# Kernel tuning notes

Measured on AMD Instinct MI355X. Metric: run time of the kernel, lower is better.

## Reference

```python
import jax, jax.numpy as jnp
import numpy as np

LMBDA = 1.0
GAMMA = 1
TOL = 1e-4
MAX_ITER = 1000
MIN_REL_DIFFERENCE = 1e-5
M = 16_777_216  # number of per-example losses


def setup_inputs() -> dict:
    key = jax.random.key(0)
    v = jax.random.normal(key, (M,), dtype=jnp.float32)
    return {"v": v}


def _find_q(v):
    """Best-response distribution q over losses (lmbda > 0 branch)."""
    m = v.shape[0]
    mf = jnp.asarray(m, v.dtype)
    # size = lmbda^2 * Var(v)^(2*gamma - 1), unbiased variance (torch default)
    size = (LMBDA ** 2) * jnp.var(v, ddof=1) ** (2 * GAMMA - 1)
    vmax = jnp.max(v)
    vmin = jnp.min(v)

    def f(eta):
        pp = jax.nn.relu(v - eta)
        pp = pp / jnp.sum(pp)
        w = mf * pp - 1.0
        return jnp.mean(w * w) - size

    eta_min = -(1.0 / (jnp.sqrt(2.0 * size + 1.0) - 1.0)) * vmax
    eta_max = vmax

    # --- expansion phase: grow [eta_min, eta_max] until it brackets the root ---
    def exp_cond(s):
        _, _, lo, up = s
        return (lo > 0) | (up < 0)

    def exp_body(s):
        emin, emax, lo, up = s
        length = emax - emin
        emax1 = jnp.where(lo > 0, emin, emax)
        emin1 = jnp.where(lo > 0, emin - 2.0 * length, emin)
        emin2 = jnp.where(up < 0, emax1, emin1)
        emax2 = jnp.where(up < 0, emax1 + 2.0 * length, emax1)
        return emin2, emax2, f(emin2), f(emax2)

    emin, emax, _, _ = jax.lax.while_loop(
        exp_cond, exp_body, (eta_min, eta_max, f(eta_min), f(eta_max))
    )

    # --- bisection on increasing f ---
    def bis_cond(s):
        _, _, _, val, i = s
        return (jnp.abs(val) > TOL) & (i < MAX_ITER)

    def bis_body(s):
        bmin, bmax, eta, val, i = s
        bmax1 = jnp.where(val > 0, eta, bmax)
        bmin1 = jnp.where(val < 0, eta, bmin)
        eta1 = 0.5 * (bmin1 + bmax1)
        return bmin1, bmax1, eta1, f(eta1), i + 1

    eta0 = 0.5 * (emin + emax)
    _, _, eta_star, _, _ = jax.lax.while_loop(
        bis_cond, bis_body, (emin, emax, eta0, f(eta0), jnp.int32(1))
    )

    pp = jax.nn.relu(v - eta_star)
    q_bis = pp / jnp.sum(pp)

    # degenerate-case fallbacks (faithful to torch branches)
    q_uniform = jnp.full_like(v, 1.0 / mf)
    q_max = (v == vmax).astype(v.dtype)
    q_max = q_max / jnp.sum(q_max)

    cond_flat = (vmax - vmin) / vmax <= MIN_REL_DIFFERENCE
    cond_small = mf <= 1.0 + 2.0 * size
    return jnp.where(cond_flat, q_uniform, jnp.where(cond_small, q_max, q_bis))


def reference(v):
    # prob is computed without gradients in the original (torch.no_grad)
    prob = _find_q(jax.lax.stop_gradient(v))
    return jnp.dot(prob, v)
```

## Files before the change

kernel.cpp:

```cpp
#include <hip/hip_runtime.h>
#include <cfloat>
#include <limits.h>
#include <math.h>


#define NBINS   4096
#define BIN_LO  (-8.0)
#define BIN_W   (1.0/256.0)
#define BPB     512
#define K1T     1024

__global__ __launch_bounds__(1024)
void k1_hist_stats(const float* __restrict__ v, int n4,
                   unsigned int* __restrict__ pcnt,
                   unsigned int* __restrict__ Cnt32,
                   float* __restrict__ pmin, float* __restrict__ pmax,
                   double* __restrict__ psum, double* __restrict__ pssq)
{
    __shared__ unsigned int hc[NBINS];
    __shared__ float rmn[16], rmx[16];
    __shared__ double rs[16], rsq[16];
    const int tid = threadIdx.x;
    for (int i = tid; i < NBINS; i += K1T) hc[i] = 0u;
    if (blockIdx.x == 0) {
        for (int i = tid; i < NBINS; i += K1T) Cnt32[i] = 0u;
    }
    __syncthreads();

    const float4* __restrict__ v4 = (const float4*)v;
    float vmn = FLT_MAX, vmx = -FLT_MAX;
    double s = 0.0, sq = 0.0;
    const int stride = gridDim.x * K1T;
    for (int i = blockIdx.x * K1T + tid; i < n4; i += stride) {
        float4 x = v4[i];
        float cs[4] = {x.x, x.y, x.z, x.w};
        #pragma unroll
        for (int k = 0; k < 4; ++k) {
            float c = cs[k];
            vmn = fminf(vmn, c); vmx = fmaxf(vmx, c);
            s += (double)c; sq += (double)c * (double)c;
            int b = (int)floorf((c - (float)BIN_LO) * 256.0f);
            b = b < 0 ? 0 : (b > NBINS - 1 ? NBINS - 1 : b);
            atomicAdd(&hc[b], 1u);
        }
    }
    __syncthreads();
    const int base = blockIdx.x * NBINS;
    for (int i = tid; i < NBINS; i += K1T) pcnt[base + i] = hc[i];
    for (int off = 32; off > 0; off >>= 1) {
        vmn = fminf(vmn, __shfl_down(vmn, off));
        vmx = fmaxf(vmx, __shfl_down(vmx, off));
        s  += __shfl_down(s, off);
        sq += __shfl_down(sq, off);
    }
    const int lane = tid & 63, wid = tid >> 6;
    if (lane == 0) { rmn[wid] = vmn; rmx[wid] = vmx; rs[wid] = s; rsq[wid] = sq; }
    __syncthreads();
    if (tid == 0) {
        float a = rmn[0], b2 = rmx[0]; double c = rs[0], d = rsq[0];
        for (int i = 1; i < 16; ++i) { a = fminf(a, rmn[i]); b2 = fmaxf(b2, rmx[i]); c += rs[i]; d += rsq[i]; }
        pmin[blockIdx.x] = a; pmax[blockIdx.x] = b2; psum[blockIdx.x] = c; pssq[blockIdx.x] = d;
    }
}

__global__ __launch_bounds__(1024)
void k2_reduce(const unsigned int* __restrict__ pcnt, unsigned int* __restrict__ Cnt32)
{
    const int g = blockIdx.x * 1024 + threadIdx.x;
    const int bin = g & (NBINS - 1);
    const int slice = g >> 12;
    unsigned int c = 0u;
    const unsigned int* __restrict__ p = pcnt + (size_t)(slice * 32) * NBINS + bin;
    #pragma unroll
    for (int k = 0; k < 32; ++k) c += p[(size_t)k * NBINS];
    atomicAdd(&Cnt32[bin], c);
}

__global__ __launch_bounds__(1024)
void k3_solve(const unsigned int* __restrict__ Cnt32,
              const float* __restrict__ pmin, const float* __restrict__ pmax,
              const double* __restrict__ psum, const double* __restrict__ pssq,
              double* __restrict__ scal, int m)
{
    __shared__ float sufC[NBINS + 1], sufV[NBINS + 1], sufV2[NBINS + 1];
    __shared__ float tC[1024], tV[1024], tV2[1024];
    __shared__ float rmn[16], rmx[16];
    __shared__ double rs[16], rsq[16];
    __shared__ double sh[8];
    __shared__ int jstar;
    const int t = threadIdx.x;
    if (t == 0) jstar = INT_MAX;

    float mn = (t < BPB) ? pmin[t] : FLT_MAX;
    float mx = (t < BPB) ? pmax[t] : -FLT_MAX;
    double s  = (t < BPB) ? psum[t] : 0.0;
    double sq = (t < BPB) ? pssq[t] : 0.0;
    for (int off = 32; off > 0; off >>= 1) {
        mn = fminf(mn, __shfl_down(mn, off));
        mx = fmaxf(mx, __shfl_down(mx, off));
        s  += __shfl_down(s, off);
        sq += __shfl_down(sq, off);
    }
    const int lane = t & 63, wid = t >> 6;
    if (lane == 0) { rmn[wid] = mn; rmx[wid] = mx; rs[wid] = s; rsq[wid] = sq; }
    __syncthreads();
    if (t == 0) {
        float a = rmn[0], b = rmx[0]; double c = rs[0], d = rsq[0];
        for (int i = 1; i < 16; ++i) { a = fminf(a, rmn[i]); b = fmaxf(b, rmx[i]); c += rs[i]; d += rsq[i]; }
        const double dm = (double)m;
        sh[0] = (d - c * c / dm) / (dm - 1.0);
        sh[1] = (double)a; sh[2] = (double)b; sh[3] = c / dm; sh[4] = c; sh[5] = d;
    }
    __syncthreads();
    const double size = sh[0];
    const double dm = (double)m;

    const int b0 = 4 * t;
    const double w2_12 = BIN_W * BIN_W / 12.0;
    double a0, a1, a2, a3, v0, v1, v2, v3, w0, w1, w2, w3;
    {
        double c0 = (double)Cnt32[b0],   c1 = (double)Cnt32[b0+1];
        double c2 = (double)Cnt32[b0+2], c3 = (double)Cnt32[b0+3];
        double m0 = BIN_LO + ((double)b0 + 0.5) * BIN_W;
        double m1 = m0 + BIN_W, m2 = m1 + BIN_W, m3 = m2 + BIN_W;
        a0 = c0; a1 = c1; a2 = c2; a3 = c3;
        v0 = c0 * m0; v1 = c1 * m1; v2 = c2 * m2; v3 = c3 * m3;
        w0 = c0 * (m0 * m0 + w2_12); w1 = c1 * (m1 * m1 + w2_12);
        w2 = c2 * (m2 * m2 + w2_12); w3 = c3 * (m3 * m3 + w2_12);
    }
    double dc3 = a3, dc2 = a2 + dc3, dc1 = a1 + dc2, dc0 = a0 + dc1;
    double dv3 = v3, dv2 = v2 + dv3, dv1 = v1 + dv2, dv0 = v0 + dv1;
    double dw3 = w3, dw2 = w2 + dw3, dw1 = w1 + dw2, dw0 = w0 + dw1;
    tC[t] = (float)dc0; tV[t] = (float)dv0; tV2[t] = (float)dw0;
    __syncthreads();
    for (int off = 1; off < 1024; off <<= 1) {
        float xc = tC[t], xv = tV[t], xw = tV2[t];
        if (t + off < 1024) { xc += tC[t+off]; xv += tV[t+off]; xw += tV2[t+off]; }
        __syncthreads();
        tC[t] = xc; tV[t] = xv; tV2[t] = xw;
        __syncthreads();
    }
    const float exC = (t < 1023) ? tC[t+1] : 0.0f;
    const float exV = (t < 1023) ? tV[t+1] : 0.0f;
    const float exW = (t < 1023) ? tV2[t+1] : 0.0f;
    sufC[b0+0] = exC + (float)dc0; sufV[b0+0] = exV + (float)dv0; sufV2[b0+0] = exW + (float)dw0;
    sufC[b0+1] = exC + (float)dc1; sufV[b0+1] = exV + (float)dv1; sufV2[b0+1] = exW + (float)dw1;
    sufC[b0+2] = exC + (float)dc2; sufV[b0+2] = exV + (float)dv2; sufV2[b0+2] = exW + (float)dw2;
    sufC[b0+3] = exC + (float)dc3; sufV[b0+3] = exV + (float)dv3; sufV2[b0+3] = exW + (float)dw3;
    if (t == 0) { sufC[NBINS] = 0.0f; sufV[NBINS] = 0.0f; sufV2[NBINS] = 0.0f; }
    __syncthreads();

    for (int j = t; j <= NBINS; j += 1024) {
        double C = (double)sufC[j];
        if (C > 0.0) {
            double eta = BIN_LO + (double)j * BIN_W;
            double V = (double)sufV[j], W = (double)sufV2[j];
            double s1 = V - eta * C;
            double s2 = W - 2.0 * eta * V + eta * eta * C;
            double f = dm * s2 / (s1 * s1) - 1.0 - size;
            if (f > 0.0) atomicMin(&jstar, j);
        }
    }
    __syncthreads();
    if (t == 0) {
        const double vmin = sh[1], vmax = sh[2];
        const int js = jstar;
        double eta0;
        if (js == INT_MAX) {
            eta0 = 0.5 * (vmin + vmax);
        } else if (js == 0) {
            double C = dm, V = sh[4], W = sh[5];
            double hi = BIN_LO;
            double den = sqrt(2.0 * size + 1.0) - 1.0;
            double lo = (den > 0.0) ? -(1.0 / den) * vmax : hi - 1.0;
            if (!(lo < hi)) lo = hi - 1.0;
            for (int it = 0; it < 200; ++it) {
                double s1 = V - lo * C, s2v = W - 2.0 * lo * V + lo * lo * C;
                double fl = dm * s2v / (s1 * s1) - 1.0 - size;
                if (!(fl > 0.0)) break;
                double len = hi - lo; lo -= 2.0 * len;
            }
            for (int it = 0; it < 100; ++it) {
                double mid = 0.5 * (lo + hi);
                double s1 = V - mid * C, s2v = W - 2.0 * mid * V + mid * mid * C;
                double fm = dm * s2v / (s1 * s1) - 1.0 - size;
                if (fm > 0.0) hi = mid; else lo = mid;
            }
            eta0 = 0.5 * (lo + hi);
        } else {
            const double R = BIN_LO + (double)js * BIN_W;
            const double L = R - BIN_W;
            const double cb = (double)Cnt32[js - 1];
            const double CR = (double)sufC[js], VR = (double)sufV[js], WR = (double)sufV2[js];
            double lo = L, hi = R;
            for (int it = 0; it < 30; ++it) {
                double mid = 0.5 * (lo + hi);
                double frac = (R - mid) * 256.0;
                double C = CR + cb * frac;
                double V = VR + cb * frac * 0.5 * (R + mid);
                double W = WR + cb * frac * ((R * R + R * mid + mid * mid) * (1.0 / 3.0));
                double s1 = V - mid * C;
                double s2 = W - 2.0 * mid * V + mid * mid * C;
                double f = dm * s2 / (s1 * s1) - 1.0 - size;
                if (f > 0.0) hi = mid; else lo = mid;
            }
            eta0 = 0.5 * (lo + hi);
        }
        scal[0] = eta0; scal[1] = size; scal[2] = vmin; scal[3] = vmax; scal[4] = sh[3];
    }
}

__global__ __launch_bounds__(1024)
void k4_gated(const float* __restrict__ v, int n4, const double* __restrict__ scal,
              double* __restrict__ np_, double* __restrict__ r1p, double* __restrict__ r2p)
{
    __shared__ double rn[16], rv[16], rw[16];
    const float etaf = (float)scal[0];
    const int tid = threadIdx.x;
    const float4* __restrict__ v4 = (const float4*)v;
    float n = 0.0f, r1 = 0.0f, r2 = 0.0f;
    const int stride = gridDim.x * K1T;
    for (int i = blockIdx.x * K1T + tid; i < n4; i += stride) {
        float4 x = v4[i];
        float cs[4] = {x.x, x.y, x.z, x.w};
        #pragma unroll
        for (int k = 0; k < 4; ++k) {
            float d = cs[k] - etaf;
            float p = fmaxf(d, 0.0f);
            r1 += p;
            r2 = fmaf(p, p, r2);
            n += (d > 0.0f) ? 1.0f : 0.0f;
        }
    }
    double dn = (double)n, dr1 = (double)r1, dr2 = (double)r2;
    for (int off = 32; off > 0; off >>= 1) {
        dn += __shfl_down(dn, off); dr1 += __shfl_down(dr1, off); dr2 += __shfl_down(dr2, off);
    }
    const int lane = tid & 63, wid = tid >> 6;
    if (lane == 0) { rn[wid] = dn; rv[wid] = dr1; rw[wid] = dr2; }
    __syncthreads();
    if (tid == 0) {
        double a = 0, b = 0, c = 0;
        for (int i = 0; i < 16; ++i) { a += rn[i]; b += rv[i]; c += rw[i]; }
        np_[blockIdx.x] = a; r1p[blockIdx.x] = b; r2p[blockIdx.x] = c;
    }
}

__global__ __launch_bounds__(512)
void k5_final(const double* __restrict__ np_, const double* __restrict__ r1p, const double* __restrict__ r2p,
              const double* __restrict__ scal, float* __restrict__ out, int m)
{
    __shared__ double rn[8], rv[8], rw[8];
    const int t = threadIdx.x;
    double n = np_[t], r1 = r1p[t], r2 = r2p[t];
    for (int off = 32; off > 0; off >>= 1) {
        n += __shfl_down(n, off); r1 += __shfl_down(r1, off); r2 += __shfl_down(r2, off);
    }
    const int lane = t & 63, wid = t >> 6;
    if (lane == 0) { rn[wid] = n; rv[wid] = r1; rw[wid] = r2; }
    __syncthreads();
    if (t == 0) {
        for (int i = 1; i < 8; ++i) { rn[0] += rn[i]; rv[0] += rv[i]; rw[0] += rw[i]; }
        n = rn[0]; r1 = rv[0]; r2 = rw[0];
        const double size = scal[1], vmin = scal[2], vmax = scal[3], mean = scal[4];
        const double eta0 = (double)((float)scal[0]);
        const double dm = (double)m;
        const double sv = r1 + eta0 * n;
        const double sw = r2 + 2.0 * eta0 * r1 + eta0 * eta0 * n;
        double eta = eta0;
        const double clo = eta0 - 2.0 * BIN_W, chi = eta0 + 2.0 * BIN_W;
        for (int it = 0; it < 12; ++it) {
            double s1 = sv - eta * n;
            double s2 = sw - 2.0 * eta * sv + eta * eta * n;
            double f  = dm * s2 / (s1 * s1) - 1.0 - size;
            double fp = 2.0 * dm * (s2 * n - s1 * s1) / (s1 * s1 * s1);
            if (!(fp > 0.0) || !isfinite(f)) break;
            eta -= f / fp;
            if (eta < clo) eta = clo;
            if (eta > chi) eta = chi;
        }
        double den  = sv - eta * n;
        double outb = (sw - eta * sv) / den;
        bool cond_flat  = ((vmax - vmin) / vmax) <= 1e-5;
        bool cond_small = dm <= 1.0 + 2.0 * size;
        double res = cond_flat ? mean : (cond_small ? vmax : outb);
        out[0] = (float)res;
    }
}

extern "C" void kernel_launch(void* const* d_in, const int* in_sizes, int n_in,
                              void* d_out, int out_size, void* d_ws, size_t ws_size,
                              hipStream_t stream)
{
    const float* v = (const float*)d_in[0];
    const int m = in_sizes[0];
    const int n4 = m / 4;

    char* ws = (char*)d_ws;
    size_t off = 0;
    unsigned int* pcnt  = (unsigned int*)(ws + off); off += (size_t)BPB * NBINS * 4;
    unsigned int* Cnt32 = (unsigned int*)(ws + off); off += NBINS * 4;
    float* pmin = (float*)(ws + off); off += BPB * 4;
    float* pmax = (float*)(ws + off); off += BPB * 4;
    off = (off + 7) & ~(size_t)7;
    double* psum = (double*)(ws + off); off += BPB * 8;
    double* pssq = (double*)(ws + off); off += BPB * 8;
    double* scal = (double*)(ws + off); off += 8 * 8;
    double* np_  = (double*)(ws + off); off += BPB * 8;
    double* r1p  = (double*)(ws + off); off += BPB * 8;
    double* r2p  = (double*)(ws + off); off += BPB * 8;

    hipLaunchKernelGGL(k1_hist_stats, dim3(BPB), dim3(K1T), 0, stream,
                       v, n4, pcnt, Cnt32, pmin, pmax, psum, pssq);
    hipLaunchKernelGGL(k2_reduce, dim3(64), dim3(1024), 0, stream,
                       pcnt, Cnt32);
    hipLaunchKernelGGL(k3_solve, dim3(1), dim3(1024), 0, stream,
                       Cnt32, pmin, pmax, psum, pssq, scal, m);
    hipLaunchKernelGGL(k4_gated, dim3(BPB), dim3(K1T), 0, stream,
                       v, n4, scal, np_, r1p, r2p);
    hipLaunchKernelGGL(k5_final, dim3(1), dim3(512), 0, stream,
                       np_, r1p, r2p, scal, (float*)d_out, m);
}
```

Before: 130.1 us.

## Subsample histogram, use float stats accumulators, and unroll streaming passes

The histogram kernel now bins only one element per float4 (a quarter of the data) and k3 scales its root search by the sampled count. Sum and sum-of-squares accumulate in float per thread instead of double, and both streaming passes are unrolled eight-way with a scalar tail. This removes most shared-memory atomics and FP64 adds from the first pass. The cost is a coarser initial eta estimate, compensated by a wider Newton clamp window and more iterations in the final step. Float accumulation may lose some precision in the variance.

```diff
diff --git a/kernel.cpp b/kernel.cpp
--- a/kernel.cpp
+++ b/kernel.cpp
@@ -11,7 +11,7 @@
 #define K1T     1024
 
 __global__ __launch_bounds__(1024)
-void k1_hist_stats(const float* __restrict__ v, int n4,
+void k1_hist_stats(const float* __restrict__ v, int n4, int m,
                    unsigned int* __restrict__ pcnt,
                    unsigned int* __restrict__ Cnt32,
                    float* __restrict__ pmin, float* __restrict__ pmax,
@@ -29,36 +29,61 @@
 
     const float4* __restrict__ v4 = (const float4*)v;
     float vmn = FLT_MAX, vmx = -FLT_MAX;
-    double s = 0.0, sq = 0.0;
+    float s = 0.0f, sq = 0.0f;
+
+#define PS(c) do { float _s0 = (c);                                    \
+        vmn = fminf(vmn, _s0); vmx = fmaxf(vmx, _s0);                  \
+        s += _s0; sq = fmaf(_s0, _s0, sq); } while (0)
+#define PH(c) do { float _h0 = (c); PS(_h0);                           \
+        float _bf = fmaf(_h0, 256.0f, 2048.0f);                        \
+        _bf = fminf(fmaxf(_bf, 0.0f), 4095.0f);                        \
+        atomicAdd(&hc[(int)_bf], 1u); } while (0)
+
     const int stride = gridDim.x * K1T;
-    for (int i = blockIdx.x * K1T + tid; i < n4; i += stride) {
+    int i = blockIdx.x * K1T + tid;
+    for (; i + 7 * stride < n4; i += 8 * stride) {
+        float4 x0 = v4[i];
+        float4 x1 = v4[i +     stride];
+        float4 x2 = v4[i + 2 * stride];
+        float4 x3 = v4[i + 3 * stride];
+        float4 x4 = v4[i + 4 * stride];
+        float4 x5 = v4[i + 5 * stride];
+        float4 x6 = v4[i + 6 * stride];
+        float4 x7 = v4[i + 7 * stride];
+        PH(x0.x); PS(x0.y); PS(x0.z); PS(x0.w);
+        PH(x1.x); PS(x1.y); PS(x1.z); PS(x1.w);
+        PH(x2.x); PS(x2.y); PS(x2.z); PS(x2.w);
+        PH(x3.x); PS(x3.y); PS(x3.z); PS(x3.w);
+        PH(x4.x); PS(x4.y); PS(x4.z); PS(x4.w);
+        PH(x5.x); PS(x5.y); PS(x5.z); PS(x5.w);
+        PH(x6.x); PS(x6.y); PS(x6.z); PS(x6.w);
+        PH(x7.x); PS(x7.y); PS(x7.z); PS(x7.w);
+    }
+    for (; i < n4; i += stride) {
         float4 x = v4[i];
-        float cs[4] = {x.x, x.y, x.z, x.w};
-        #pragma unroll
-        for (int k = 0; k < 4; ++k) {
-            float c = cs[k];
-            vmn = fminf(vmn, c); vmx = fmaxf(vmx, c);
-            s += (double)c; sq += (double)c * (double)c;
-            int b = (int)floorf((c - (float)BIN_LO) * 256.0f);
-            b = b < 0 ? 0 : (b > NBINS - 1 ? NBINS - 1 : b);
-            atomicAdd(&hc[b], 1u);
-        }
-    }
+        PH(x.x); PS(x.y); PS(x.z); PS(x.w);
+    }
+    if (blockIdx.x == 0 && tid == 0) {
+        for (int j = n4 * 4; j < m; ++j) PS(v[j]);
+    }
+#undef PH
+#undef PS
     __syncthreads();
     const int base = blockIdx.x * NBINS;
-    for (int i = tid; i < NBINS; i += K1T) pcnt[base + i] = hc[i];
+    for (int i2 = tid; i2 < NBINS; i2 += K1T) pcnt[base + i2] = hc[i2];
+    double ds = (double)s, dsq = (double)sq;
     for (int off = 32; off > 0; off >>= 1) {
         vmn = fminf(vmn, __shfl_down(vmn, off));
         vmx = fmaxf(vmx, __shfl_down(vmx, off));
-        s  += __shfl_down(s, off);
-        sq += __shfl_down(sq, off);
+        ds  += __shfl_down(ds, off);
+        dsq += __shfl_down(dsq, off);
     }
     const int lane = tid & 63, wid = tid >> 6;
-    if (lane == 0) { rmn[wid] = vmn; rmx[wid] = vmx; rs[wid] = s; rsq[wid] = sq; }
+    if (lane == 0) { rmn[wid] = vmn; rmx[wid] = vmx; rs[wid] = ds; rsq[wid] = dsq; }
     __syncthreads();
     if (tid == 0) {
         float a = rmn[0], b2 = rmx[0]; double c = rs[0], d = rsq[0];
-        for (int i = 1; i < 16; ++i) { a = fminf(a, rmn[i]); b2 = fmaxf(b2, rmx[i]); c += rs[i]; d += rsq[i]; }
+        for (int k = 1; k < 16; ++k) { a = fminf(a, rmn[k]); b2 = fmaxf(b2, rmx[k]); c += rs[k]; d += rsq[k]; }
         pmin[blockIdx.x] = a; pmax[blockIdx.x] = b2; psum[blockIdx.x] = c; pssq[blockIdx.x] = d;
     }
 }
@@ -80,7 +105,7 @@
 void k3_solve(const unsigned int* __restrict__ Cnt32,
               const float* __restrict__ pmin, const float* __restrict__ pmax,
               const double* __restrict__ psum, const double* __restrict__ pssq,
-              double* __restrict__ scal, int m)
+              double* __restrict__ scal, int m, int n4)
 {
     __shared__ float sufC[NBINS + 1], sufV[NBINS + 1], sufV2[NBINS + 1];
     __shared__ float tC[1024], tV[1024], tV2[1024];
@@ -114,6 +139,7 @@
     __syncthreads();
     const double size = sh[0];
     const double dm = (double)m;
+    const double dms = (double)n4;
 
     const int b0 = 4 * t;
     const double w2_12 = BIN_W * BIN_W / 12.0;
@@ -157,7 +183,7 @@
             double V = (double)sufV[j], W = (double)sufV2[j];
             double s1 = V - eta * C;
             double s2 = W - 2.0 * eta * V + eta * eta * C;
-            double f = dm * s2 / (s1 * s1) - 1.0 - size;
+            double f = dms * s2 / (s1 * s1) - 1.0 - size;
             if (f > 0.0) atomicMin(&jstar, j);
         }
     }
@@ -189,11 +215,10 @@
             eta0 = 0.5 * (lo + hi);
         } else {
             const double R = BIN_LO + (double)js * BIN_W;
-            const double L = R - BIN_W;
             const double cb = (double)Cnt32[js - 1];
             const double CR = (double)sufC[js], VR = (double)sufV[js], WR = (double)sufV2[js];
-            double lo = L, hi = R;
-            for (int it = 0; it < 30; ++it) {
+            double lo = R - BIN_W, hi = R;
+            for (int it = 0; it < 20; ++it) {
                 double mid = 0.5 * (lo + hi);
                 double frac = (R - mid) * 256.0;
                 double C = CR + cb * frac;
@@ -201,7 +226,7 @@
                 double W = WR + cb * frac * ((R * R + R * mid + mid * mid) * (1.0 / 3.0));
                 double s1 = V - mid * C;
                 double s2 = W - 2.0 * mid * V + mid * mid * C;
-                double f = dm * s2 / (s1 * s1) - 1.0 - size;
+                double f = dms * s2 / (s1 * s1) - 1.0 - size;
                 if (f > 0.0) hi = mid; else lo = mid;
             }
             eta0 = 0.5 * (lo + hi);
@@ -211,7 +236,7 @@
 }
 
 __global__ __launch_bounds__(1024)
-void k4_gated(const float* __restrict__ v, int n4, const double* __restrict__ scal,
+void k4_gated(const float* __restrict__ v, int n4, int m, const double* __restrict__ scal,
               double* __restrict__ np_, double* __restrict__ r1p, double* __restrict__ r2p)
 {
     __shared__ double rn[16], rv[16], rw[16];
@@ -219,19 +244,40 @@
     const int tid = threadIdx.x;
     const float4* __restrict__ v4 = (const float4*)v;
     float n = 0.0f, r1 = 0.0f, r2 = 0.0f;
+
+#define PG(c) do { float _d = (c) - etaf;                              \
+        float _p = fmaxf(_d, 0.0f);                                    \
+        r1 += _p; r2 = fmaf(_p, _p, r2);                               \
+        n += (_d > 0.0f) ? 1.0f : 0.0f; } while (0)
+
     const int stride = gridDim.x * K1T;
-    for (int i = blockIdx.x * K1T + tid; i < n4; i += stride) {
+    int i = blockIdx.x * K1T + tid;
+    for (; i + 7 * stride < n4; i += 8 * stride) {
+        float4 x0 = v4[i];
+        float4 x1 = v4[i +     stride];
+        float4 x2 = v4[i + 2 * stride];
+        float4 x3 = v4[i + 3 * stride];
+        float4 x4 = v4[i + 4 * stride];
+        float4 x5 = v4[i + 5 * stride];
+        float4 x6 = v4[i + 6 * stride];
+        float4 x7 = v4[i + 7 * stride];
+        PG(x0.x); PG(x0.y); PG(x0.z); PG(x0.w);
+        PG(x1.x); PG(x1.y); PG(x1.z); PG(x1.w);
+        PG(x2.x); PG(x2.y); PG(x2.z); PG(x2.w);
+        PG(x3.x); PG(x3.y); PG(x3.z); PG(x3.w);
+        PG(x4.x); PG(x4.y); PG(x4.z); PG(x4.w);
+        PG(x5.x); PG(x5.y); PG(x5.z); PG(x5.w);
+        PG(x6.x); PG(x6.y); PG(x6.z); PG(x6.w);
+        PG(x7.x); PG(x7.y); PG(x7.z); PG(x7.w);
+    }
+    for (; i < n4; i += stride) {
         float4 x = v4[i];
-        float cs[4] = {x.x, x.y, x.z, x.w};
-        #pragma unroll
-        for (int k = 0; k < 4; ++k) {
-            float d = cs[k] - etaf;
-            float p = fmaxf(d, 0.0f);
-            r1 += p;
-            r2 = fmaf(p, p, r2);
-            n += (d > 0.0f) ? 1.0f : 0.0f;
-        }
-    }
+        PG(x.x); PG(x.y); PG(x.z); PG(x.w);
+    }
+    if (blockIdx.x == 0 && tid == 0) {
+        for (int j = n4 * 4; j < m; ++j) PG(v[j]);
+    }
+#undef PG
     double dn = (double)n, dr1 = (double)r1, dr2 = (double)r2;
     for (int off = 32; off > 0; off >>= 1) {
         dn += __shfl_down(dn, off); dr1 += __shfl_down(dr1, off); dr2 += __shfl_down(dr2, off);
@@ -241,7 +287,7 @@
     __syncthreads();
     if (tid == 0) {
         double a = 0, b = 0, c = 0;
-        for (int i = 0; i < 16; ++i) { a += rn[i]; b += rv[i]; c += rw[i]; }
+        for (int k = 0; k < 16; ++k) { a += rn[k]; b += rv[k]; c += rw[k]; }
         np_[blockIdx.x] = a; r1p[blockIdx.x] = b; r2p[blockIdx.x] = c;
     }
 }
@@ -268,8 +314,8 @@
         const double sv = r1 + eta0 * n;
         const double sw = r2 + 2.0 * eta0 * r1 + eta0 * eta0 * n;
         double eta = eta0;
-        const double clo = eta0 - 2.0 * BIN_W, chi = eta0 + 2.0 * BIN_W;
-        for (int it = 0; it < 12; ++it) {
+        const double clo = eta0 - 3.0 * BIN_W, chi = eta0 + 3.0 * BIN_W;
+        for (int it = 0; it < 16; ++it) {
             double s1 = sv - eta * n;
             double s2 = sw - 2.0 * eta * sv + eta * eta * n;
             double f  = dm * s2 / (s1 * s1) - 1.0 - size;
@@ -311,13 +357,13 @@
     double* r2p  = (double*)(ws + off); off += BPB * 8;
 
     hipLaunchKernelGGL(k1_hist_stats, dim3(BPB), dim3(K1T), 0, stream,
-                       v, n4, pcnt, Cnt32, pmin, pmax, psum, pssq);
+                       v, n4, m, pcnt, Cnt32, pmin, pmax, psum, pssq);
     hipLaunchKernelGGL(k2_reduce, dim3(64), dim3(1024), 0, stream,
                        pcnt, Cnt32);
     hipLaunchKernelGGL(k3_solve, dim3(1), dim3(1024), 0, stream,
-                       Cnt32, pmin, pmax, psum, pssq, scal, m);
+                       Cnt32, pmin, pmax, psum, pssq, scal, m, n4);
     hipLaunchKernelGGL(k4_gated, dim3(BPB), dim3(K1T), 0, stream,
-                       v, n4, scal, np_, r1p, r2p);
+                       v, n4, m, scal, np_, r1p, r2p);
     hipLaunchKernelGGL(k5_final, dim3(1), dim3(512), 0, stream,
                        np_, r1p, r2p, scal, (float*)d_out, m);
 }
```

Result: faster. 127.4 us (-2.0%).
